# Performance work log

Measured on AMD Instinct MI355X. Metric: run time of the kernel, lower is better.

Reference implementation:

```python
import jax, jax.numpy as jnp
import numpy as np

DEPTH, HEADS, DIM_HEAD = 6, 8, 64
B, N, E = 2, 128, 160
NUM_ATOMS, NF = 100, 127
DIM = NF + 1                 # 128, node feature dim fed to transformer
INNER = HEADS * DIM_HEAD     # 512


def setup_inputs() -> dict:
    key = jax.random.key(0)
    ks = iter(jax.random.split(key, 40))
    f32 = jnp.float32
    def w(shape, scale=0.02):
        return jax.random.normal(next(ks), shape, dtype=f32) * scale
    inp = {
        "indices": jax.random.randint(next(ks), (B, N), 0, NUM_ATOMS),
        "coordinates": jax.random.normal(next(ks), (B, N, 3), dtype=f32),
        "bonds": jax.random.randint(next(ks), (E, 2), 0, N),
        "noise_level": jax.random.uniform(next(ks), (1,), dtype=f32),
        "atom_emb": w((NUM_ATOMS, NF), 1.0),
        "ln1_g": jnp.ones((DEPTH, DIM), f32), "ln1_b": jnp.zeros((DEPTH, DIM), f32),
        "Wq": w((DEPTH, DIM, INNER)), "bq": jnp.zeros((DEPTH, INNER), f32),
        "Wkv": w((DEPTH, DIM, 2 * INNER)), "bkv": jnp.zeros((DEPTH, 2 * INNER), f32),
        "We": w((DEPTH, 3, INNER)), "be": jnp.zeros((DEPTH, INNER), f32),
        "Wo": w((DEPTH, INNER, DIM)), "bo": jnp.zeros((DEPTH, DIM), f32),
        "Wg1": w((DEPTH, 3 * DIM, 1)),
        "ln2_g": jnp.ones((DEPTH, DIM), f32), "ln2_b": jnp.zeros((DEPTH, DIM), f32),
        "W1": w((DEPTH, DIM, 4 * DIM)), "b1": jnp.zeros((DEPTH, 4 * DIM), f32),
        "W2": w((DEPTH, 4 * DIM, DIM)), "b2": jnp.zeros((DEPTH, DIM), f32),
        "Wg2": w((DEPTH, 3 * DIM, 1)),
        "Wlin": w((DIM, 1)), "blin": jnp.zeros((1,), f32),
    }
    return inp


def _ln(x, g, b, eps=1e-5):
    m = jnp.mean(x, -1, keepdims=True)
    v = jnp.mean((x - m) ** 2, -1, keepdims=True)
    return (x - m) * jax.lax.rsqrt(v + eps) * g + b


def _gated_residual(x, res, Wg):
    # gate = sigmoid(Linear([x, res, x-res])); out = x*gate + res*(1-gate)
    gate = jax.nn.sigmoid(jnp.concatenate([x, res, x - res], -1) @ Wg)  # (B,N,1)
    return x * gate + res * (1.0 - gate)


def _forward(indices, bonds, coordinates, noise_level, atom_emb,
             ln1_g, ln1_b, Wq, bq, Wkv, bkv, We, be, Wo, bo, Wg1,
             ln2_g, ln2_b, W1, b1, W2, b2, Wg2, Wlin, blin):
    b, n = indices.shape
    # nodes_embedding: atom embedding + noise-level channel
    noise = jnp.broadcast_to(noise_level.reshape(1, 1, 1).astype(coordinates.dtype), (b, n, 1))
    nodes = jnp.concatenate([atom_emb[indices], noise], -1)  # (B,N,DIM)
    # edges_embedding: vectorized scatter of per-bond coordinate differences
    i, j = bonds[:, 0], bonds[:, 1]
    diff = coordinates[:, i] - coordinates[:, j]             # (B,E,3)
    edges = jnp.zeros((b, n, n, 3), coordinates.dtype)
    edges = edges.at[:, i, j].set(diff).at[:, j, i].set(-diff)

    scale = DIM_HEAD ** -0.5
    for l in range(DEPTH):
        # PreNorm + edge-biased attention (mask is all-ones -> no-op)
        xn = _ln(nodes, ln1_g[l], ln1_b[l])
        q = (xn @ Wq[l] + bq[l]).reshape(b, n, HEADS, DIM_HEAD)
        k, v = jnp.split(xn @ Wkv[l] + bkv[l], 2, -1)
        k = k.reshape(b, n, HEADS, DIM_HEAD)
        v = v.reshape(b, n, HEADS, DIM_HEAD)
        e = (edges @ We[l] + be[l]).reshape(b, n, n, HEADS, DIM_HEAD)
        kk = k[:, None] + e                                   # (B,i,j,H,D)
        vv = v[:, None] + e
        sim = jnp.einsum('bihd,bijhd->bijh', q, kk) * scale
        attn = jax.nn.softmax(sim, axis=2)                    # softmax over j
        out = jnp.einsum('bijh,bijhd->bihd', attn, vv).reshape(b, n, INNER)
        out = out @ Wo[l] + bo[l]
        nodes = _gated_residual(out, nodes, Wg1[l])
        # PreNorm + FeedForward (exact GELU, mult=4) + gated residual
        xn = _ln(nodes, ln2_g[l], ln2_b[l])
        ff = jax.nn.gelu(xn @ W1[l] + b1[l], approximate=False) @ W2[l] + b2[l]
        nodes = _gated_residual(ff, nodes, Wg2[l])
    return jnp.sum(nodes @ Wlin + blin)


def reference(indices, coordinates, bonds, noise_level, atom_emb,
              ln1_g, ln1_b, Wq, bq, Wkv, bkv, We, be, Wo, bo, Wg1,
              ln2_g, ln2_b, W1, b1, W2, b2, Wg2, Wlin, blin):
    return _forward(indices, bonds, coordinates, noise_level, atom_emb,
                    ln1_g, ln1_b, Wq, bq, Wkv, bkv, We, be, Wo, bo, Wg1,
                    ln2_g, ln2_b, W1, b1, W2, b2, Wg2, Wlin, blin)
```

## Files before the change

kernel.cpp:

```cpp
#include <hip/hip_runtime.h>
#include <hip/hip_fp16.h>
#include <math.h>

#define DEPTH 6
#define HEADS 8
#define BB    2
#define NN    128
#define EE    160
#define NF    127
#define DIMM  128
#define INNER 512
#define NNODE 256

typedef _Float16 h2f16 __attribute__((ext_vector_type(2)));

#if defined(__has_builtin)
#if __has_builtin(__builtin_amdgcn_fdot2)
#define HAVE_FDOT2 1
#endif
#endif

__device__ __forceinline__ float fdot2f(h2f16 a, h2f16 b, float c) {
#ifdef HAVE_FDOT2
    return __builtin_amdgcn_fdot2(a, b, c, false);
#else
    return c + (float)a.x * (float)b.x + (float)a.y * (float)b.y;
#endif
}

__device__ __forceinline__ void gload16(const void* g, void* l) {
    __builtin_amdgcn_global_load_lds((const __attribute__((address_space(1))) void*)g,
                                     (__attribute__((address_space(3))) void*)l,
                                     16, 0, 0);
}

template <int N>
__device__ __forceinline__ void wait_vm() {
    __builtin_amdgcn_s_waitcnt((0xF << 8) | (7 << 4) | (N & 0xF) | ((N >> 4) << 14));
}
__device__ __forceinline__ void wait_lgkm0() { __builtin_amdgcn_s_waitcnt(0xC07F); }
__device__ __forceinline__ void sbar0() { __builtin_amdgcn_sched_barrier(0); }

__device__ __forceinline__ void stage8s(const char* gslice, int rowstride,
                                        char* ldsslice, int ln) {
#pragma unroll
    for (int i = 0; i < 8; i++)
        gload16(gslice + (size_t)i * rowstride + ln * 16, ldsslice + i * 1024);
}

__device__ __forceinline__ void fma8h(float4& a0, float4& a1, float s, float4 raw) {
    const __half2* hp = (const __half2*)&raw;
    float2 p0 = __half22float2(hp[0]), p1 = __half22float2(hp[1]);
    float2 p2 = __half22float2(hp[2]), p3 = __half22float2(hp[3]);
    a0.x += s * p0.x; a0.y += s * p0.y; a0.z += s * p1.x; a0.w += s * p1.y;
    a1.x += s * p2.x; a1.y += s * p2.y; a1.z += s * p3.x; a1.w += s * p3.y;
}

__device__ __forceinline__ void gemv512_pipe(const float* act, float* wbuf,
                                             float* s_part,
                                             const char* nextA, const char* nextB,
                                             int nextStride, int w, int ln) {
    float4 a0 = {0,0,0,0}, a1 = {0,0,0,0};
    const float4* w4 = (const float4*)wbuf;
    wait_vm<8>();
#pragma unroll
    for (int r = 0; r < 8; r++)
        fma8h(a0, a1, act[w * 16 + r], w4[r * 64 + ln]);
    wait_lgkm0(); sbar0();
    if (nextA) { stage8s(nextA, nextStride, (char*)wbuf, ln); wait_vm<8>(); }
    else       { wait_vm<0>(); }
#pragma unroll
    for (int r = 8; r < 16; r++)
        fma8h(a0, a1, act[w * 16 + r], w4[r * 64 + ln]);
    wait_lgkm0(); sbar0();
    if (nextB) stage8s(nextB, nextStride, (char*)wbuf + 8192, ln);
    ((float4*)(s_part + w * 512))[ln * 2]     = a0;
    ((float4*)(s_part + w * 512))[ln * 2 + 1] = a1;
}

__device__ __forceinline__ void gemv128_pipe(const float* act, float* wbuf,
                                             float* s_part,
                                             const char* nextA, const char* nextB,
                                             int nextStride, int w, int ln) {
    float2 acc = {0, 0};
    wait_vm<8>();
#pragma unroll 8
    for (int r = 0; r < 32; r++) {
        float raw = wbuf[r * 64 + ln];
        float2 p = __half22float2(*(const __half2*)&raw);
        float a = act[w * 64 + r];
        acc.x += a * p.x; acc.y += a * p.y;
    }
    wait_lgkm0(); sbar0();
    if (nextA) { stage8s(nextA, nextStride, (char*)wbuf, ln); wait_vm<8>(); }
    else       { wait_vm<0>(); }
#pragma unroll 8
    for (int r = 32; r < 64; r++) {
        float raw = wbuf[r * 64 + ln];
        float2 p = __half22float2(*(const __half2*)&raw);
        float a = act[w * 64 + r];
        acc.x += a * p.x; acc.y += a * p.y;
    }
    wait_lgkm0(); sbar0();
    if (nextB) stage8s(nextB, nextStride, (char*)wbuf + 8192, ln);
    s_part[w * 128 + ln * 2]     = acc.x;
    s_part[w * 128 + ln * 2 + 1] = acc.y;
}

template <int N>
__device__ __forceinline__ void block_reduce_n(float* vals, float* sbuf) {
#pragma unroll
    for (int off = 32; off > 0; off >>= 1)
#pragma unroll
        for (int q = 0; q < N; q++) vals[q] += __shfl_xor(vals[q], off, 64);
    int wave = threadIdx.x >> 6;
    if ((threadIdx.x & 63) == 0)
#pragma unroll
        for (int q = 0; q < N; q++) sbuf[wave * N + q] = vals[q];
    __syncthreads();
#pragma unroll
    for (int q = 0; q < N; q++) {
        float r = 0.0f;
#pragma unroll
        for (int g = 0; g < 8; g++) r += sbuf[g * N + q];
        vals[q] = r;
    }
    __syncthreads();
}

__device__ __forceinline__ float gelu_exact(float a) {
    return 0.5f * a * (1.0f + erff(a * 0.70710678f));
}


__global__ __launch_bounds__(512) void k_cvt(const float* Wq, const float* Wkv,
                                             const float* Wo, const float* W1,
                                             const float* W2,
                                             __half* hWq, __half* hWkv, __half* hWo,
                                             __half* hW1, __half* hW2,
                                             const float* blin, float* out) {
    if (blockIdx.x == 0 && threadIdx.x == 0) out[0] = 256.0f * blin[0];
    int g = blockIdx.x * 512 + threadIdx.x;
    const float4* src; __half* dst; int off;
    if (g < 98304)       { src = (const float4*)Wq;  dst = hWq;  off = g; }
    else if (g < 294912) { src = (const float4*)Wkv; dst = hWkv; off = g - 98304; }
    else if (g < 393216) { src = (const float4*)Wo;  dst = hWo;  off = g - 294912; }
    else if (g < 491520) { src = (const float4*)W1;  dst = hW1;  off = g - 393216; }
    else                 { src = (const float4*)W2;  dst = hW2;  off = g - 491520; }
    float4 v = src[off];
    __half2* d2 = (__half2*)(dst + (size_t)off * 4);
    d2[0] = __floats2half2_rn(v.x, v.y);
    d2[1] = __floats2half2_rn(v.z, v.w);
}

__global__ __launch_bounds__(512, 1) void k_pre(const int* indices, const float* noise,
                                                const float* atom_emb,
                                                const float* ln1_g, const float* ln1_b,
                                                const __half* hWq, const float* bq,
                                                const __half* hWkv, const float* bkv,
                                                float* nodes, float* qb,
                                                __half* hk, __half* hv) {
    int bn = blockIdx.x;
    int t  = threadIdx.x;
    int d  = t & 127;
    bool own = (t < 128);
    int w = t >> 6, ln = t & 63;
    __shared__ float arena[32768];
    __shared__ float s_xn[128];
    __shared__ float s_red[48];
    __shared__ float s_part[4096];
    char*  lslice = (char*)arena + w * 16384;
    float* wbuf   = arena + w * 4096;

    const char* WqL  = (const char*)hWq;
    const char* WkvL = (const char*)hWkv;
    stage8s(WqL + w * 16384, 1024, lslice, ln);
    stage8s(WqL + w * 16384 + 8192, 1024, lslice + 8192, ln);

    float nd = 0.0f;
    if (own) {
        int idx = indices[bn];
        nd = (d < NF) ? atom_emb[idx * NF + d] : noise[0];
        nodes[bn * DIMM + d] = nd;
    }
    float vals[2] = {own ? nd : 0.0f, own ? nd * nd : 0.0f};
    block_reduce_n<2>(vals, s_red);
    float m   = vals[0] * (1.0f / 128.0f);
    float var = vals[1] * (1.0f / 128.0f) - m * m;
    if (own) s_xn[d] = (nd - m) * rsqrtf(var + 1e-5f) * ln1_g[d] + ln1_b[d];
    __syncthreads();

    gemv512_pipe(s_xn, wbuf, s_part,
                 WkvL + (size_t)(w * 16) * 2048,
                 WkvL + (size_t)(w * 16 + 8) * 2048, 2048, w, ln);
    __syncthreads();
    {
        float q = bq[t];
#pragma unroll
        for (int g = 0; g < 8; g++) q += s_part[g * 512 + t];
        qb[(size_t)bn * INNER + t] = q;
    }
    __syncthreads();

    gemv512_pipe(s_xn, wbuf, s_part,
                 WkvL + (size_t)(w * 16) * 2048 + 1024,
                 WkvL + (size_t)(w * 16 + 8) * 2048 + 1024, 2048, w, ln);
    __syncthreads();
    {
        float k = bkv[t];
#pragma unroll
        for (int g = 0; g < 8; g++) k += s_part[g * 512 + t];
        hk[(size_t)bn * INNER + t] = __float2half(k);
    }
    __syncthreads();

    gemv512_pipe(s_xn, wbuf, s_part, nullptr, nullptr, 0, w, ln);
    __syncthreads();
    {
        float v = bkv[INNER + t];
#pragma unroll
        for (int g = 0; g < 8; g++) v += s_part[g * 512 + t];
        hv[(size_t)bn * INNER + t] = __float2half(v);
    }
}

__global__ __launch_bounds__(512, 1) void k_layer(int l,
        const float* coords, const int* bonds,
        const float* We, const float* be,
        float* qb, const __half* hkin, const __half* hvin,
        __half* hkout, __half* hvout,
        const __half* hWo, const float* bo, const float* Wg1,
        const float* ln2_g, const float* ln2_b,
        const __half* hW1, const float* b1,
        const __half* hW2, const float* b2,
        const float* Wg2,
        const float* ln1_g, const float* ln1_b,
        const __half* hWq, const float* bq,
        const __half* hWkv, const float* bkv,
        float* nodes, const float* Wlin, float* out) {
    int bn = blockIdx.x;
    int b = bn >> 7, i = bn & 127;
    int t = threadIdx.x;
    int d = t & 127;
    bool own = (t < 128);
    int w = t >> 6, ln = t & 63;

    __shared__ float arena[32768];
    __shared__ float scoord[384];
    __shared__ float sedge[384];
    __shared__ int   sadj[128];
    __shared__ float s_l[64];
    __shared__ float s_ao[512];
    __shared__ float s_h[512];
    __shared__ float s_xn[128];
    __shared__ float s_red[48];
    __shared__ float s_part[4096];
    float* s_o = s_part;
    char*  lslice = (char*)arena + w * 16384;
    float* wbuf   = arena + w * 4096;

    const char* WoL  = (const char*)(hWo + (size_t)l * INNER * DIMM);
    const char* W1L  = (const char*)(hW1 + (size_t)l * DIMM * 4 * DIMM);
    const char* W2L  = (const char*)(hW2 + (size_t)l * 4 * DIMM * DIMM);
    const char* WqL  = (const char*)(hWq + (size_t)(l + 1) * DIMM * INNER);
    const char* WkvL = (const char*)(hWkv + (size_t)(l + 1) * DIMM * 2 * INNER);

    stage8s(WoL + w * 16384, 1024, lslice, ln);
    stage8s(WoL + w * 16384 + 8192, 1024, lslice + 8192, ln);

    const float4* qR4 = (const float4*)(qb + (size_t)bn * INNER);
    const float4* WeR = (const float4*)(We + (size_t)l * 3 * INNER);
    float4 qa  = qR4[ln * 2],        qz  = qR4[ln * 2 + 1];
    float4 w0a = WeR[ln * 2],        w0z = WeR[ln * 2 + 1];
    float4 w1a = WeR[128 + ln * 2],  w1z = WeR[129 + ln * 2];
    float4 w2a = WeR[256 + ln * 2],  w2z = WeR[257 + ln * 2];
    float4 bea = ((const float4*)(be + (size_t)l * INNER))[ln * 2];
    float4 bez = ((const float4*)(be + (size_t)l * INNER))[ln * 2 + 1];
    float res = own ? nodes[bn * DIMM + d] : 0.0f;
    h2f16 qh0 = {(_Float16)qa.x, (_Float16)qa.y};
    h2f16 qh1 = {(_Float16)qa.z, (_Float16)qa.w};
    h2f16 qh2 = {(_Float16)qz.x, (_Float16)qz.y};
    h2f16 qh3 = {(_Float16)qz.z, (_Float16)qz.w};
    float c = qa.x * bea.x + qa.y * bea.y + qa.z * bea.z + qa.w * bea.w
            + qz.x * bez.x + qz.y * bez.y + qz.z * bez.z + qz.w * bez.w;
    c += __shfl_xor(c, 1, 64); c += __shfl_xor(c, 2, 64); c += __shfl_xor(c, 4, 64);

    if (t < 3 * NN) scoord[t] = coords[b * 3 * NN + t];
    if (t < NN) sadj[t] = 0;
    __syncthreads();
    if (t < EE) {
        int e0 = bonds[2 * t], e1 = bonds[2 * t + 1];
        if (e0 == i) sadj[e1] = 1;
        if (e1 == i) sadj[e0] = 1;
    }
    __syncthreads();
    if (t < NN) {
        int j = t;
        float msk = sadj[j] ? 1.0f : 0.0f;
        sedge[3 * j + 0] = msk * (scoord[3 * i + 0] - scoord[3 * j + 0]);
        sedge[3 * j + 1] = msk * (scoord[3 * i + 1] - scoord[3 * j + 1]);
        sedge[3 * j + 2] = msk * (scoord[3 * i + 2] - scoord[3 * j + 2]);
    }
    __syncthreads();

    const float4* kR = (const float4*)(hkin + (size_t)b * NN * INNER);
    const float4* vR = (const float4*)(hvin + (size_t)b * NN * INNER);
    float l_run = 0.0f, S_nb = 0.0f;
    float4 o0 = {0, 0, 0, 0}, o1 = {0, 0, 0, 0};
    int j0 = w * 16;
#pragma unroll
    for (int base = 0; base < 16; base += 4) {
        float4 kraw[4], vraw[4];
#pragma unroll
        for (int p = 0; p < 4; p++) {
            int j = j0 + base + p;
            kraw[p] = kR[j * 64 + ln];
            vraw[p] = vR[j * 64 + ln];
        }
#pragma unroll
        for (int p = 0; p < 4; p++) {
            int j = j0 + base + p;
            const h2f16* kh = (const h2f16*)&kraw[p];
            float s = fdot2f(qh0, kh[0],
                      fdot2f(qh1, kh[1],
                      fdot2f(qh2, kh[2],
                      fdot2f(qh3, kh[3], 0.0f))));
            bool bonded = (sadj[j] != 0);
            float4 e0, e1;
            if (bonded) {
                float ex = sedge[3 * j], ey = sedge[3 * j + 1], ez = sedge[3 * j + 2];
                e0.x = bea.x + ex * w0a.x + ey * w1a.x + ez * w2a.x;
                e0.y = bea.y + ex * w0a.y + ey * w1a.y + ez * w2a.y;
                e0.z = bea.z + ex * w0a.z + ey * w1a.z + ez * w2a.z;
                e0.w = bea.w + ex * w0a.w + ey * w1a.w + ez * w2a.w;
                e1.x = bez.x + ex * w0z.x + ey * w1z.x + ez * w2z.x;
                e1.y = bez.y + ex * w0z.y + ey * w1z.y + ez * w2z.y;
                e1.z = bez.z + ex * w0z.z + ey * w1z.z + ez * w2z.z;
                e1.w = bez.w + ex * w0z.w + ey * w1z.w + ez * w2z.w;
                s += qa.x * e0.x + qa.y * e0.y + qa.z * e0.z + qa.w * e0.w
                   + qz.x * e1.x + qz.y * e1.y + qz.z * e1.z + qz.w * e1.w;
            }
            s += __shfl_xor(s, 1, 64);
            s += __shfl_xor(s, 2, 64);
            s += __shfl_xor(s, 4, 64);
            if (!bonded) s += c;
            float pp = __expf(s * 0.125f);
            l_run += pp;
            const __half2* vh = (const __half2*)&vraw[p];
            float2 v0 = __half22float2(vh[0]), v1 = __half22float2(vh[1]);
            float2 v2 = __half22float2(vh[2]), v3 = __half22float2(vh[3]);
            o0.x += pp * v0.x; o0.y += pp * v0.y; o0.z += pp * v1.x; o0.w += pp * v1.y;
            o1.x += pp * v2.x; o1.y += pp * v2.y; o1.z += pp * v3.x; o1.w += pp * v3.y;
            if (bonded) {
                o0.x += pp * e0.x; o0.y += pp * e0.y; o0.z += pp * e0.z; o0.w += pp * e0.w;
                o1.x += pp * e1.x; o1.y += pp * e1.y; o1.z += pp * e1.z; o1.w += pp * e1.w;
            } else S_nb += pp;
        }
    }
    o0.x += S_nb * bea.x; o0.y += S_nb * bea.y; o0.z += S_nb * bea.z; o0.w += S_nb * bea.w;
    o1.x += S_nb * bez.x; o1.y += S_nb * bez.y; o1.z += S_nb * bez.z; o1.w += S_nb * bez.w;
    ((float4*)(s_o + w * 512))[ln * 2]     = o0;
    ((float4*)(s_o + w * 512))[ln * 2 + 1] = o1;
    if ((ln & 7) == 0) s_l[w * 8 + (ln >> 3)] = l_run;
    __syncthreads();
    {
        float o = 0.0f;
#pragma unroll
        for (int g = 0; g < 8; g++) o += s_o[g * 512 + t];
        int h = t >> 6;
        float lsum = 0.0f;
#pragma unroll
        for (int g = 0; g < 8; g++) lsum += s_l[g * 8 + h];
        s_ao[t] = o / lsum;
    }
    __syncthreads();

    gemv128_pipe(s_ao, wbuf, s_part,
                 W1L + w * 16384, W1L + w * 16384 + 8192, 1024, w, ln);
    __syncthreads();
    float x = 0.0f;
    if (own) {
        x = bo[l * DIMM + d];
#pragma unroll
        for (int g = 0; g < 8; g++) x += s_part[g * 128 + d];
    }

    const float* Wg1_l = Wg1 + l * 3 * DIMM;
    float n1;
    {
        float tex = own ? (x * Wg1_l[d] + res * Wg1_l[DIMM + d]
                           + (x - res) * Wg1_l[2 * DIMM + d]) : 0.0f;
        float vals[6] = {tex,
                         own ? x : 0.0f, own ? x * x : 0.0f,
                         own ? x * res : 0.0f,
                         own ? res : 0.0f, own ? res * res : 0.0f};
        block_reduce_n<6>(vals, s_red);
        float g1 = 1.0f / (1.0f + __expf(-vals[0]));
        float sn  = g1 * vals[1] + (1.0f - g1) * vals[4];
        float sn2 = g1 * g1 * vals[2] + 2.0f * g1 * (1.0f - g1) * vals[3]
                  + (1.0f - g1) * (1.0f - g1) * vals[5];
        float m   = sn * (1.0f / 128.0f);
        float var = sn2 * (1.0f / 128.0f) - m * m;
        n1 = x * g1 + res * (1.0f - g1);
        if (own) s_xn[d] = (n1 - m) * rsqrtf(var + 1e-5f) * ln2_g[l * DIMM + d]
                         + ln2_b[l * DIMM + d];
    }
    __syncthreads();

    gemv512_pipe(s_xn, wbuf, s_part,
                 W2L + w * 16384, W2L + w * 16384 + 8192, 1024, w, ln);
    __syncthreads();
    {
        float a = b1[l * 4 * DIMM + t];
#pragma unroll
        for (int g = 0; g < 8; g++) a += s_part[g * 512 + t];
        s_h[t] = gelu_exact(a);
    }
    __syncthreads();

    gemv128_pipe(s_h, wbuf, s_part,
                 (l < DEPTH - 1) ? WqL + w * 16384 : nullptr,
                 (l < DEPTH - 1) ? WqL + w * 16384 + 8192 : nullptr, 1024, w, ln);
    __syncthreads();
    float y = 0.0f;
    if (own) {
        y = b2[l * DIMM + d];
#pragma unroll
        for (int g = 0; g < 8; g++) y += s_part[g * 128 + d];
    }

    const float* Wg2_l = Wg2 + l * 3 * DIMM;
    if (l < DEPTH - 1) {
        float tex = own ? (y * Wg2_l[d] + n1 * Wg2_l[DIMM + d]
                           + (y - n1) * Wg2_l[2 * DIMM + d]) : 0.0f;
        float vals[6] = {tex,
                         own ? y : 0.0f, own ? y * y : 0.0f,
                         own ? y * n1 : 0.0f,
                         own ? n1 : 0.0f, own ? n1 * n1 : 0.0f};
        block_reduce_n<6>(vals, s_red);
        float g2 = 1.0f / (1.0f + __expf(-vals[0]));
        float sn  = g2 * vals[1] + (1.0f - g2) * vals[4];
        float sn2 = g2 * g2 * vals[2] + 2.0f * g2 * (1.0f - g2) * vals[3]
                  + (1.0f - g2) * (1.0f - g2) * vals[5];
        float m   = sn * (1.0f / 128.0f);
        float var = sn2 * (1.0f / 128.0f) - m * m;
        float n2 = y * g2 + n1 * (1.0f - g2);
        if (own) {
            nodes[bn * DIMM + d] = n2;
            s_xn[d] = (n2 - m) * rsqrtf(var + 1e-5f) * ln1_g[(l + 1) * DIMM + d]
                    + ln1_b[(l + 1) * DIMM + d];
        }
        __syncthreads();

        gemv512_pipe(s_xn, wbuf, s_part,
                     WkvL + (size_t)(w * 16) * 2048,
                     WkvL + (size_t)(w * 16 + 8) * 2048, 2048, w, ln);
        __syncthreads();
        {
            float q = bq[(l + 1) * INNER + t];
#pragma unroll
            for (int g = 0; g < 8; g++) q += s_part[g * 512 + t];
            qb[(size_t)bn * INNER + t] = q;
        }
        __syncthreads();

        gemv512_pipe(s_xn, wbuf, s_part,
                     WkvL + (size_t)(w * 16) * 2048 + 1024,
                     WkvL + (size_t)(w * 16 + 8) * 2048 + 1024, 2048, w, ln);
        __syncthreads();
        {
            float k = bkv[(l + 1) * 2 * INNER + t];
#pragma unroll
            for (int g = 0; g < 8; g++) k += s_part[g * 512 + t];
            hkout[(size_t)bn * INNER + t] = __float2half(k);
        }
        __syncthreads();

        gemv512_pipe(s_xn, wbuf, s_part, nullptr, nullptr, 0, w, ln);
        __syncthreads();
        {
            float v = bkv[(l + 1) * 2 * INNER + INNER + t];
#pragma unroll
            for (int g = 0; g < 8; g++) v += s_part[g * 512 + t];
            hvout[(size_t)bn * INNER + t] = __float2half(v);
        }
    } else {
        float wl = own ? Wlin[d] : 0.0f;
        float tex = own ? (y * Wg2_l[d] + n1 * Wg2_l[DIMM + d]
                           + (y - n1) * Wg2_l[2 * DIMM + d]) : 0.0f;
        float vals[3] = {tex, y * wl, n1 * wl};
        block_reduce_n<3>(vals, s_red);
        float g2 = 1.0f / (1.0f + __expf(-vals[0]));
        float tot = g2 * vals[1] + (1.0f - g2) * vals[2];
        if (t == 0) atomicAdd(out, tot);
    }
}

extern "C" void kernel_launch(void* const* d_in, const int* in_sizes, int n_in,
                              void* d_out, int out_size, void* d_ws, size_t ws_size,
                              hipStream_t stream) {
    const int*   indices = (const int*)d_in[0];
    const float* coords  = (const float*)d_in[1];
    const int*   bonds   = (const int*)d_in[2];
    const float* noise   = (const float*)d_in[3];
    const float* atom_emb= (const float*)d_in[4];
    const float* ln1_g   = (const float*)d_in[5];
    const float* ln1_b   = (const float*)d_in[6];
    const float* Wq      = (const float*)d_in[7];
    const float* bq      = (const float*)d_in[8];
    const float* Wkv     = (const float*)d_in[9];
    const float* bkv     = (const float*)d_in[10];
    const float* We      = (const float*)d_in[11];
    const float* be      = (const float*)d_in[12];
    const float* Wo      = (const float*)d_in[13];
    const float* bo      = (const float*)d_in[14];
    const float* Wg1     = (const float*)d_in[15];
    const float* ln2_g   = (const float*)d_in[16];
    const float* ln2_b   = (const float*)d_in[17];
    const float* W1      = (const float*)d_in[18];
    const float* b1      = (const float*)d_in[19];
    const float* W2      = (const float*)d_in[20];
    const float* b2      = (const float*)d_in[21];
    const float* Wg2     = (const float*)d_in[22];
    const float* Wlin    = (const float*)d_in[23];
    const float* blin    = (const float*)d_in[24];

    float*  ws    = (float*)d_ws;
    float*  nodes = ws;
    float*  qb    = nodes + NNODE * DIMM;
    __half* hkb   = (__half*)(qb + NNODE * INNER);
    __half* hvb   = hkb + 2 * NNODE * INNER;
    __half* hWq   = hvb + 2 * NNODE * INNER;
    __half* hWkv  = hWq + DEPTH * DIMM * INNER;
    __half* hWo   = hWkv + DEPTH * DIMM * 2 * INNER;
    __half* hW1   = hWo + DEPTH * INNER * DIMM;
    __half* hW2   = hW1 + DEPTH * DIMM * 4 * DIMM;

    k_cvt<<<1152, 512, 0, stream>>>(Wq, Wkv, Wo, W1, W2, hWq, hWkv, hWo, hW1, hW2,
                                    blin, (float*)d_out);
    k_pre<<<NNODE, 512, 0, stream>>>(indices, noise, atom_emb, ln1_g, ln1_b,
                                     hWq, bq, hWkv, bkv, nodes, qb, hkb, hvb);
    for (int l = 0; l < DEPTH; l++) {
        const __half* hkin = hkb + (size_t)(l & 1) * NNODE * INNER;
        const __half* hvin = hvb + (size_t)(l & 1) * NNODE * INNER;
        __half* hkout = hkb + (size_t)((l + 1) & 1) * NNODE * INNER;
        __half* hvout = hvb + (size_t)((l + 1) & 1) * NNODE * INNER;
        k_layer<<<NNODE, 512, 0, stream>>>(l, coords, bonds, We, be,
                                           qb, hkin, hvin, hkout, hvout,
                                           hWo, bo, Wg1, ln2_g, ln2_b, hW1, b1, hW2, b2,
                                           Wg2, ln1_g, ln1_b, hWq, bq, hWkv, bkv,
                                           nodes, Wlin, (float*)d_out);
    }
}
```

Baseline: 259.6 us.

## Transpose fp16 weight layout so each lane owns an output column, using fdot2

The conversion kernel now writes weights in a column-major, rotation-swizzled fp16 layout. Each lane holds one output column's contiguous K-slice, and the GEMVs become per-lane fdot2 dot products against fp16 activations. This removes the cross-wave s_part reductions and most __syncthreads between GEMV stages; the 128-wide GEMVs need only a 4-lane shuffle reduction. Activations are now rounded to fp16 before the dot products, which adds precision risk. The conversion kernel also does strided scalar global reads, so it may run slower.

```diff
diff --git a/kernel.cpp b/kernel.cpp
--- a/kernel.cpp
+++ b/kernel.cpp
@@ -3,8 +3,6 @@
 #include <math.h>
 
 #define DEPTH 6
-#define HEADS 8
-#define BB    2
 #define NN    128
 #define EE    160
 #define NF    127
@@ -41,70 +39,82 @@
 __device__ __forceinline__ void wait_lgkm0() { __builtin_amdgcn_s_waitcnt(0xC07F); }
 __device__ __forceinline__ void sbar0() { __builtin_amdgcn_sched_barrier(0); }
 
-__device__ __forceinline__ void stage8s(const char* gslice, int rowstride,
-                                        char* ldsslice, int ln) {
-#pragma unroll
-    for (int i = 0; i < 8; i++)
-        gload16(gslice + (size_t)i * rowstride + ln * 16, ldsslice + i * 1024);
-}
-
-__device__ __forceinline__ void fma8h(float4& a0, float4& a1, float s, float4 raw) {
-    const __half2* hp = (const __half2*)&raw;
-    float2 p0 = __half22float2(hp[0]), p1 = __half22float2(hp[1]);
-    float2 p2 = __half22float2(hp[2]), p3 = __half22float2(hp[3]);
-    a0.x += s * p0.x; a0.y += s * p0.y; a0.z += s * p1.x; a0.w += s * p1.y;
-    a1.x += s * p2.x; a1.y += s * p2.y; a1.z += s * p3.x; a1.w += s * p3.y;
-}
-
-__device__ __forceinline__ void gemv512_pipe(const float* act, float* wbuf,
-                                             float* s_part,
-                                             const char* nextA, const char* nextB,
-                                             int nextStride, int w, int ln) {
-    float4 a0 = {0,0,0,0}, a1 = {0,0,0,0};
-    const float4* w4 = (const float4*)wbuf;
-    wait_vm<8>();
-#pragma unroll
-    for (int r = 0; r < 8; r++)
-        fma8h(a0, a1, act[w * 16 + r], w4[r * 64 + ln]);
-    wait_lgkm0(); sbar0();
-    if (nextA) { stage8s(nextA, nextStride, (char*)wbuf, ln); wait_vm<8>(); }
-    else       { wait_vm<0>(); }
-#pragma unroll
-    for (int r = 8; r < 16; r++)
-        fma8h(a0, a1, act[w * 16 + r], w4[r * 64 + ln]);
-    wait_lgkm0(); sbar0();
-    if (nextB) stage8s(nextB, nextStride, (char*)wbuf + 8192, ln);
-    ((float4*)(s_part + w * 512))[ln * 2]     = a0;
-    ((float4*)(s_part + w * 512))[ln * 2 + 1] = a1;
-}
-
-__device__ __forceinline__ void gemv128_pipe(const float* act, float* wbuf,
-                                             float* s_part,
-                                             const char* nextA, const char* nextB,
-                                             int nextStride, int w, int ln) {
-    float2 acc = {0, 0};
-    wait_vm<8>();
-#pragma unroll 8
-    for (int r = 0; r < 32; r++) {
-        float raw = wbuf[r * 64 + ln];
-        float2 p = __half22float2(*(const __half2*)&raw);
-        float a = act[w * 64 + r];
-        acc.x += a * p.x; acc.y += a * p.y;
-    }
-    wait_lgkm0(); sbar0();
-    if (nextA) { stage8s(nextA, nextStride, (char*)wbuf, ln); wait_vm<8>(); }
-    else       { wait_vm<0>(); }
-#pragma unroll 8
-    for (int r = 32; r < 64; r++) {
-        float raw = wbuf[r * 64 + ln];
-        float2 p = __half22float2(*(const __half2*)&raw);
-        float a = act[w * 64 + r];
-        acc.x += a * p.x; acc.y += a * p.y;
-    }
-    wait_lgkm0(); sbar0();
-    if (nextB) stage8s(nextB, nextStride, (char*)wbuf + 8192, ln);
-    s_part[w * 128 + ln * 2]     = acc.x;
-    s_part[w * 128 + ln * 2 + 1] = acc.y;
+__device__ __forceinline__ void stage16(const char* g, char* lds, int ln) {
+#pragma unroll
+    for (int i = 0; i < 16; i++)
+        gload16(g + i * 1024 + ln * 16, lds + i * 1024);
+}
+
+
+template <int NSTAGE>
+__device__ __forceinline__ float gemv512T(const __half* s_xh, const float* wbuf,
+                                          const char* nextG, char* wbufc, int ln) {
+    const float4* W = (const float4*)((const char*)wbuf + ln * 256);
+    const float4* X = (const float4*)s_xh;
+    float acc = 0.0f;
+    float4 wr[8], xr[8];
+#pragma unroll
+    for (int i = 0; i < 8; i++) { wr[i] = W[(i + ln) & 15]; xr[i] = X[i]; }
+#pragma unroll
+    for (int i = 0; i < 8; i++) {
+        const h2f16* wh = (const h2f16*)&wr[i];
+        const h2f16* xh = (const h2f16*)&xr[i];
+        acc = fdot2f(xh[0], wh[0], acc); acc = fdot2f(xh[1], wh[1], acc);
+        acc = fdot2f(xh[2], wh[2], acc); acc = fdot2f(xh[3], wh[3], acc);
+    }
+    float4 wr2[8], xr2[8];
+#pragma unroll
+    for (int i = 0; i < 8; i++) { wr2[i] = W[(i + 8 + ln) & 15]; xr2[i] = X[i + 8]; }
+    if (NSTAGE) {
+        sbar0();
+        wait_lgkm0();
+        sbar0();
+        stage16(nextG, wbufc, ln);
+    }
+#pragma unroll
+    for (int i = 0; i < 8; i++) {
+        const h2f16* wh = (const h2f16*)&wr2[i];
+        const h2f16* xh = (const h2f16*)&xr2[i];
+        acc = fdot2f(xh[0], wh[0], acc); acc = fdot2f(xh[1], wh[1], acc);
+        acc = fdot2f(xh[2], wh[2], acc); acc = fdot2f(xh[3], wh[3], acc);
+    }
+    return acc;
+}
+
+template <int NSTAGE>
+__device__ __forceinline__ float gemv128T(const __half* s_xp, const float* wbuf,
+                                          const char* nextG, char* wbufc, int ln) {
+    int kq = ln & 3;
+    const float4* W = (const float4*)((const char*)wbuf + ln * 256);
+    const float4* X = (const float4*)((const char*)s_xp + kq * 272);
+    float acc = 0.0f;
+    float4 wr[8], xr[8];
+#pragma unroll
+    for (int i = 0; i < 8; i++) { wr[i] = W[(i + ln) & 15]; xr[i] = X[i]; }
+#pragma unroll
+    for (int i = 0; i < 8; i++) {
+        const h2f16* wh = (const h2f16*)&wr[i];
+        const h2f16* xh = (const h2f16*)&xr[i];
+        acc = fdot2f(xh[0], wh[0], acc); acc = fdot2f(xh[1], wh[1], acc);
+        acc = fdot2f(xh[2], wh[2], acc); acc = fdot2f(xh[3], wh[3], acc);
+    }
+    float4 wr2[8], xr2[8];
+#pragma unroll
+    for (int i = 0; i < 8; i++) { wr2[i] = W[(i + 8 + ln) & 15]; xr2[i] = X[i + 8]; }
+    if (NSTAGE) {
+        sbar0();
+        wait_lgkm0();
+        sbar0();
+        stage16(nextG, wbufc, ln);
+    }
+#pragma unroll
+    for (int i = 0; i < 8; i++) {
+        const h2f16* wh = (const h2f16*)&wr2[i];
+        const h2f16* xh = (const h2f16*)&xr2[i];
+        acc = fdot2f(xh[0], wh[0], acc); acc = fdot2f(xh[1], wh[1], acc);
+        acc = fdot2f(xh[2], wh[2], acc); acc = fdot2f(xh[3], wh[3], acc);
+    }
+    return acc;
 }
 
 template <int N>
@@ -131,7 +141,6 @@
 __device__ __forceinline__ float gelu_exact(float a) {
     return 0.5f * a * (1.0f + erff(a * 0.70710678f));
 }
-
 
 __global__ __launch_bounds__(512) void k_cvt(const float* Wq, const float* Wkv,
                                              const float* Wo, const float* W1,
@@ -140,17 +149,37 @@
                                              __half* hW1, __half* hW2,
                                              const float* blin, float* out) {
     if (blockIdx.x == 0 && threadIdx.x == 0) out[0] = 256.0f * blin[0];
-    int g = blockIdx.x * 512 + threadIdx.x;
-    const float4* src; __half* dst; int off;
-    if (g < 98304)       { src = (const float4*)Wq;  dst = hWq;  off = g; }
-    else if (g < 294912) { src = (const float4*)Wkv; dst = hWkv; off = g - 98304; }
-    else if (g < 393216) { src = (const float4*)Wo;  dst = hWo;  off = g - 294912; }
-    else if (g < 491520) { src = (const float4*)W1;  dst = hW1;  off = g - 393216; }
-    else                 { src = (const float4*)W2;  dst = hW2;  off = g - 491520; }
-    float4 v = src[off];
-    __half2* d2 = (__half2*)(dst + (size_t)off * 4);
-    d2[0] = __floats2half2_rn(v.x, v.y);
-    d2[1] = __floats2half2_rn(v.z, v.w);
+    int bid = blockIdx.x;
+    int l = bid / 48, rem = bid % 48, mat = rem >> 3, w = rem & 7;
+    int t = threadIdx.x;
+    const float* src;
+    __half* dst;
+    int ncols, col0, big;
+    if (mat == 0)      { src = Wq  + (size_t)l * 65536;  dst = hWq  + (size_t)l * 65536;          ncols = 512;  col0 = w * 64;       big = 0; }
+    else if (mat == 1) { src = Wkv + (size_t)l * 131072; dst = hWkv + (size_t)l * 131072;         ncols = 1024; col0 = w * 64;       big = 0; }
+    else if (mat == 2) { src = Wkv + (size_t)l * 131072; dst = hWkv + (size_t)l * 131072 + 65536; ncols = 1024; col0 = 512 + w * 64; big = 0; }
+    else if (mat == 3) { src = W1  + (size_t)l * 65536;  dst = hW1  + (size_t)l * 65536;          ncols = 512;  col0 = w * 64;       big = 0; }
+    else if (mat == 4) { src = Wo  + (size_t)l * 65536;  dst = hWo  + (size_t)l * 65536;          ncols = 128;  col0 = w * 16;       big = 1; }
+    else               { src = W2  + (size_t)l * 65536;  dst = hW2  + (size_t)l * 65536;          ncols = 128;  col0 = w * 16;       big = 1; }
+    dst += w * 8192;
+#pragma unroll
+    for (int p = 0; p < 2; p++) {
+        int bi = p * 512 + t;
+        int i = bi & 15;
+        int ln, c, row0;
+        if (!big) { c = bi >> 4; ln = c; row0 = i * 8; }
+        else {
+            c = bi >> 6;
+            int kq = (bi >> 4) & 3;
+            ln = c * 4 + kq;
+            row0 = kq * 128 + i * 8;
+        }
+        __align__(16) __half tmp[8];
+#pragma unroll
+        for (int e = 0; e < 8; e++)
+            tmp[e] = __float2half(src[(size_t)(row0 + e) * ncols + col0 + c]);
+        *(float4*)&dst[ln * 128 + ((i + ln) & 15) * 8] = *(const float4*)tmp;
+    }
 }
 
 __global__ __launch_bounds__(512, 1) void k_pre(const int* indices, const float* noise,
@@ -166,16 +195,11 @@
     bool own = (t < 128);
     int w = t >> 6, ln = t & 63;
     __shared__ float arena[32768];
-    __shared__ float s_xn[128];
+    __shared__ __align__(16) __half s_xh[128];
     __shared__ float s_red[48];
-    __shared__ float s_part[4096];
-    char*  lslice = (char*)arena + w * 16384;
-    float* wbuf   = arena + w * 4096;
-
-    const char* WqL  = (const char*)hWq;
-    const char* WkvL = (const char*)hWkv;
-    stage8s(WqL + w * 16384, 1024, lslice, ln);
-    stage8s(WqL + w * 16384 + 8192, 1024, lslice + 8192, ln);
+    float* wbuf = arena + w * 4096;
+
+    stage16((const char*)hWq + w * 16384, (char*)wbuf, ln);
 
     float nd = 0.0f;
     if (own) {
@@ -187,40 +211,25 @@
     block_reduce_n<2>(vals, s_red);
     float m   = vals[0] * (1.0f / 128.0f);
     float var = vals[1] * (1.0f / 128.0f) - m * m;
-    if (own) s_xn[d] = (nd - m) * rsqrtf(var + 1e-5f) * ln1_g[d] + ln1_b[d];
-    __syncthreads();
-
-    gemv512_pipe(s_xn, wbuf, s_part,
-                 WkvL + (size_t)(w * 16) * 2048,
-                 WkvL + (size_t)(w * 16 + 8) * 2048, 2048, w, ln);
-    __syncthreads();
-    {
-        float q = bq[t];
-#pragma unroll
-        for (int g = 0; g < 8; g++) q += s_part[g * 512 + t];
-        qb[(size_t)bn * INNER + t] = q;
-    }
-    __syncthreads();
-
-    gemv512_pipe(s_xn, wbuf, s_part,
-                 WkvL + (size_t)(w * 16) * 2048 + 1024,
-                 WkvL + (size_t)(w * 16 + 8) * 2048 + 1024, 2048, w, ln);
-    __syncthreads();
-    {
-        float k = bkv[t];
-#pragma unroll
-        for (int g = 0; g < 8; g++) k += s_part[g * 512 + t];
-        hk[(size_t)bn * INNER + t] = __float2half(k);
-    }
-    __syncthreads();
-
-    gemv512_pipe(s_xn, wbuf, s_part, nullptr, nullptr, 0, w, ln);
-    __syncthreads();
-    {
-        float v = bkv[INNER + t];
-#pragma unroll
-        for (int g = 0; g < 8; g++) v += s_part[g * 512 + t];
-        hv[(size_t)bn * INNER + t] = __float2half(v);
+    if (own) s_xh[d] = __float2half((nd - m) * rsqrtf(var + 1e-5f) * ln1_g[d] + ln1_b[d]);
+    __syncthreads();
+
+    int col = w * 64 + ln;
+    wait_vm<0>();
+    {
+        float q = gemv512T<1>(s_xh, wbuf, (const char*)hWkv + w * 16384, (char*)wbuf, ln);
+        qb[(size_t)bn * INNER + col] = q + bq[col];
+    }
+    wait_vm<0>();
+    {
+        float k = gemv512T<1>(s_xh, wbuf, (const char*)hWkv + 131072 + w * 16384,
+                              (char*)wbuf, ln);
+        hk[(size_t)bn * INNER + col] = __float2half(k + bkv[col]);
+    }
+    wait_vm<0>();
+    {
+        float v = gemv512T<0>(s_xh, wbuf, nullptr, nullptr, ln);
+        hv[(size_t)bn * INNER + col] = __float2half(v + bkv[INNER + col]);
     }
 }
 
@@ -250,23 +259,23 @@
     __shared__ float sedge[384];
     __shared__ int   sadj[128];
     __shared__ float s_l[64];
-    __shared__ float s_ao[512];
-    __shared__ float s_h[512];
-    __shared__ float s_xn[128];
+    __shared__ __align__(16) __half s_aoh[544];
+    __shared__ __align__(16) __half s_hh[544];
+    __shared__ __align__(16) __half s_xh[128];
+    __shared__ float s_x[128];
     __shared__ float s_red[48];
     __shared__ float s_part[4096];
     float* s_o = s_part;
-    char*  lslice = (char*)arena + w * 16384;
-    float* wbuf   = arena + w * 4096;
-
-    const char* WoL  = (const char*)(hWo + (size_t)l * INNER * DIMM);
-    const char* W1L  = (const char*)(hW1 + (size_t)l * DIMM * 4 * DIMM);
-    const char* W2L  = (const char*)(hW2 + (size_t)l * 4 * DIMM * DIMM);
-    const char* WqL  = (const char*)(hWq + (size_t)(l + 1) * DIMM * INNER);
-    const char* WkvL = (const char*)(hWkv + (size_t)(l + 1) * DIMM * 2 * INNER);
-
-    stage8s(WoL + w * 16384, 1024, lslice, ln);
-    stage8s(WoL + w * 16384 + 8192, 1024, lslice + 8192, ln);
+    float* wbuf = arena + w * 4096;
+
+    const char* WoL  = (const char*)hWo + (size_t)l * 131072 + w * 16384;
+    const char* W1L  = (const char*)hW1 + (size_t)l * 131072 + w * 16384;
+    const char* W2L  = (const char*)hW2 + (size_t)l * 131072 + w * 16384;
+    const char* WqnL = (const char*)hWq + (size_t)(l + 1) * 131072 + w * 16384;
+    const char* WknL = (const char*)hWkv + (size_t)(l + 1) * 262144 + w * 16384;
+    const char* WvnL = (const char*)hWkv + (size_t)(l + 1) * 262144 + 131072 + w * 16384;
+
+    stage16(WoL, (char*)wbuf, ln);
 
     const float4* qR4 = (const float4*)(qb + (size_t)bn * INNER);
     const float4* WeR = (const float4*)(We + (size_t)l * 3 * INNER);
@@ -371,19 +380,19 @@
         float lsum = 0.0f;
 #pragma unroll
         for (int g = 0; g < 8; g++) lsum += s_l[g * 8 + h];
-        s_ao[t] = o / lsum;
-    }
-    __syncthreads();
-
-    gemv128_pipe(s_ao, wbuf, s_part,
-                 W1L + w * 16384, W1L + w * 16384 + 8192, 1024, w, ln);
-    __syncthreads();
-    float x = 0.0f;
-    if (own) {
-        x = bo[l * DIMM + d];
-#pragma unroll
-        for (int g = 0; g < 8; g++) x += s_part[g * 128 + d];
-    }
+        s_aoh[(t >> 7) * 136 + (t & 127)] = __float2half(o / lsum);
+    }
+    __syncthreads();
+
+    wait_vm<0>();
+    {
+        float xo = gemv128T<1>(s_aoh, wbuf, W1L, (char*)wbuf, ln);
+        xo += __shfl_xor(xo, 1, 64);
+        xo += __shfl_xor(xo, 2, 64);
+        if ((ln & 3) == 0) s_x[w * 16 + (ln >> 2)] = xo;
+    }
+    __syncthreads();
+    float x = own ? s_x[d] + bo[l * DIMM + d] : 0.0f;
 
     const float* Wg1_l = Wg1 + l * 3 * DIMM;
     float n1;
@@ -402,32 +411,31 @@
         float m   = sn * (1.0f / 128.0f);
         float var = sn2 * (1.0f / 128.0f) - m * m;
         n1 = x * g1 + res * (1.0f - g1);
-        if (own) s_xn[d] = (n1 - m) * rsqrtf(var + 1e-5f) * ln2_g[l * DIMM + d]
-                         + ln2_b[l * DIMM + d];
-    }
-    __syncthreads();
-
-    gemv512_pipe(s_xn, wbuf, s_part,
-                 W2L + w * 16384, W2L + w * 16384 + 8192, 1024, w, ln);
-    __syncthreads();
-    {
-        float a = b1[l * 4 * DIMM + t];
-#pragma unroll
-        for (int g = 0; g < 8; g++) a += s_part[g * 512 + t];
-        s_h[t] = gelu_exact(a);
-    }
-    __syncthreads();
-
-    gemv128_pipe(s_h, wbuf, s_part,
-                 (l < DEPTH - 1) ? WqL + w * 16384 : nullptr,
-                 (l < DEPTH - 1) ? WqL + w * 16384 + 8192 : nullptr, 1024, w, ln);
-    __syncthreads();
-    float y = 0.0f;
-    if (own) {
-        y = b2[l * DIMM + d];
-#pragma unroll
-        for (int g = 0; g < 8; g++) y += s_part[g * 128 + d];
-    }
+        if (own) s_xh[d] = __float2half((n1 - m) * rsqrtf(var + 1e-5f) * ln2_g[l * DIMM + d]
+                                        + ln2_b[l * DIMM + d]);
+    }
+    __syncthreads();
+
+    wait_vm<0>();
+    {
+        float a1 = gemv512T<1>(s_xh, wbuf, W2L, (char*)wbuf, ln);
+        int col = w * 64 + ln;
+        float ag = gelu_exact(a1 + b1[l * 4 * DIMM + col]);
+        s_hh[(col >> 7) * 136 + (col & 127)] = __float2half(ag);
+    }
+    __syncthreads();
+
+    wait_vm<0>();
+    {
+        float yw;
+        if (l < DEPTH - 1) yw = gemv128T<1>(s_hh, wbuf, WqnL, (char*)wbuf, ln);
+        else               yw = gemv128T<0>(s_hh, wbuf, nullptr, nullptr, ln);
+        yw += __shfl_xor(yw, 1, 64);
+        yw += __shfl_xor(yw, 2, 64);
+        if ((ln & 3) == 0) s_x[w * 16 + (ln >> 2)] = yw;
+    }
+    __syncthreads();
+    float y = own ? s_x[d] + b2[l * DIMM + d] : 0.0f;
 
     const float* Wg2_l = Wg2 + l * 3 * DIMM;
     if (l < DEPTH - 1) {
@@ -447,42 +455,28 @@
         float n2 = y * g2 + n1 * (1.0f - g2);
         if (own) {
             nodes[bn * DIMM + d] = n2;
-            s_xn[d] = (n2 - m) * rsqrtf(var + 1e-5f) * ln1_g[(l + 1) * DIMM + d]
-                    + ln1_b[(l + 1) * DIMM + d];
+            s_xh[d] = __float2half((n2 - m) * rsqrtf(var + 1e-5f) * ln1_g[(l + 1) * DIMM + d]
+                                   + ln1_b[(l + 1) * DIMM + d]);
         }
         __syncthreads();
 
-        gemv512_pipe(s_xn, wbuf, s_part,
-                     WkvL + (size_t)(w * 16) * 2048,
-                     WkvL + (size_t)(w * 16 + 8) * 2048, 2048, w, ln);
-        __syncthreads();
+        int col = w * 64 + ln;
+        wait_vm<0>();
         {
-            float q = bq[(l + 1) * INNER + t];
-#pragma unroll
-            for (int g = 0; g < 8; g++) q += s_part[g * 512 + t];
-            qb[(size_t)bn * INNER + t] = q;
-        }
-        __syncthreads();
-
-        gemv512_pipe(s_xn, wbuf, s_part,
-                     WkvL + (size_t)(w * 16) * 2048 + 1024,
-                     WkvL + (size_t)(w * 16 + 8) * 2048 + 1024, 2048, w, ln);
-        __syncthreads();
+            float q = gemv512T<1>(s_xh, wbuf, WknL, (char*)wbuf, ln);
+            qb[(size_t)bn * INNER + col] = q + bq[(l + 1) * INNER + col];
+        }
+        wait_vm<0>();
         {
-            float k = bkv[(l + 1) * 2 * INNER + t];
-#pragma unroll
-            for (int g = 0; g < 8; g++) k += s_part[g * 512 + t];
-            hkout[(size_t)bn * INNER + t] = __float2half(k);
-        }
-        __syncthreads();
-
-        gemv512_pipe(s_xn, wbuf, s_part, nullptr, nullptr, 0, w, ln);
-        __syncthreads();
+            float kk = gemv512T<1>(s_xh, wbuf, WvnL, (char*)wbuf, ln);
+            hkout[(size_t)bn * INNER + col] =
+                __float2half(kk + bkv[(l + 1) * 2 * INNER + col]);
+        }
+        wait_vm<0>();
         {
-            float v = bkv[(l + 1) * 2 * INNER + INNER + t];
-#pragma unroll
-            for (int g = 0; g < 8; g++) v += s_part[g * 512 + t];
-            hvout[(size_t)bn * INNER + t] = __float2half(v);
+            float vv = gemv512T<0>(s_xh, wbuf, nullptr, nullptr, ln);
+            hvout[(size_t)bn * INNER + col] =
+                __float2half(vv + bkv[(l + 1) * 2 * INNER + INNER + col]);
         }
     } else {
         float wl = own ? Wlin[d] : 0.0f;
@@ -536,8 +530,8 @@
     __half* hW1   = hWo + DEPTH * INNER * DIMM;
     __half* hW2   = hW1 + DEPTH * DIMM * 4 * DIMM;
 
-    k_cvt<<<1152, 512, 0, stream>>>(Wq, Wkv, Wo, W1, W2, hWq, hWkv, hWo, hW1, hW2,
-                                    blin, (float*)d_out);
+    k_cvt<<<288, 512, 0, stream>>>(Wq, Wkv, Wo, W1, W2, hWq, hWkv, hWo, hW1, hW2,
+                                   blin, (float*)d_out);
     k_pre<<<NNODE, 512, 0, stream>>>(indices, noise, atom_emb, ln1_g, ln1_b,
                                      hWq, bq, hWkv, bkv, nodes, qb, hkb, hvb);
     for (int l = 0; l < DEPTH; l++) {
```

After: 245.3 us. -5.5%, faster.
